# Kernel optimization log

Measured on AMD Instinct MI355X. Metric: run time of the kernel, lower is better.

The kernel has to match this reference:

```python
import jax, jax.numpy as jnp
import numpy as np

B, L, V = 4, 1024, 1280
N_EMBD, N_BIN, N_HID = 768, 8, 32
HORIZON = 10.0


def setup_inputs() -> dict:
    key = jax.random.key(0)
    k_h, k_age, k_gap, k_tgt, k_w1, k_w2 = jax.random.split(key, 6)
    h = jax.random.normal(k_h, (B, L, N_EMBD), dtype=jnp.float32)
    # ages increase along a trajectory; gaps in [0, 2) years
    age = jnp.sort(jax.random.uniform(k_age, (B, L), dtype=jnp.float32) * 80.0, axis=-1)
    targets_age = age + jax.random.uniform(k_gap, (B, L), dtype=jnp.float32) * 2.0
    delta_t = targets_age - age  # passed to forward but unused (as in torch source)
    targets = jax.random.randint(k_tgt, (B, L), 0, V, dtype=jnp.int32)
    W1 = jax.random.normal(k_w1, (N_EMBD, N_BIN * N_HID), dtype=jnp.float32) * 0.02
    W2 = jax.random.normal(k_w2, (N_HID, V), dtype=jnp.float32) * 0.02
    return {"h": h, "age": age, "targets_age": targets_age, "delta_t": delta_t,
            "targets": targets, "W1": W1, "W2": W2}


def _time_to_event(age, targets_age, targets):
    # delta_full[b,i,j] = targets_age[b,j] - age[b,i]
    delta_full = targets_age[:, None, :] - age[:, :, None]  # (B,L,L)
    i_idx = jnp.arange(L)
    # torch.triu(diagonal=0): keep targets[b,j] where j>=i, else 0
    upper = (i_idx[None, :] >= i_idx[:, None])  # (L,L) mask, col>=row
    targets_exp = jnp.where(upper[None, :, :], targets[:, None, :], 0)  # (B,L,L)
    # scatter-reduce amin of position index j into vocab slot targets_exp[b,i,j]
    # sentinel L plays the role of torch's -1 (min over srcs ignores it; src<=L-1)
    b_ix = jnp.arange(B)[:, None, None]
    r_ix = i_idx[None, :, None]
    src = jnp.broadcast_to(i_idx[None, None, :], (B, L, L)).astype(jnp.int32)
    token_index = jnp.full((B, L, V), L, dtype=jnp.int32)
    token_index = token_index.at[b_ix, r_ix, targets_exp].min(src)
    no_event = token_index == L
    token_index = jnp.where(no_event, L - 1, token_index)  # (B,L,V)
    tte = jnp.take_along_axis(delta_full, token_index, axis=-1)  # (B,L,V)
    return tte, no_event, token_index


def reference(h, age, targets_age, delta_t, targets, W1, W2):
    # two dense projections: (B,L,E) -> (B,L,n_bin,n_hid) -> (B,L,n_bin,V)
    x = jnp.einsum('ble,eo->blo', h, W1).reshape(B, L, N_BIN, N_HID)
    logits = jnp.einsum('blnh,hv->blnv', x, W2)
    tte, no_event, _ = _time_to_event(age, targets_age, targets)
    edges = jnp.linspace(0.0, HORIZON, N_BIN + 1)
    lo = edges[:-1][None, None, :, None]
    hi = edges[1:][None, None, :, None]
    t = tte[:, :, None, :]  # (B,L,1,V)
    censor_mask = ((t >= lo) & (t < hi)) | no_event[:, :, None, :]  # (B,L,n_bin,V)
    return logits, tte, censor_mask
```

## Files before the change

kernel.cpp:

```cpp
#include <hip/hip_runtime.h>
#include <hip/hip_bf16.h>

#define B_   4
#define L_   1024
#define V_   1280
#define NE_  768
#define NB_  8
#define NH_  32
#define NO_  (NB_*NH_)
#define BL_  (B_*L_)
#define M2_  (BL_*NB_)

typedef __attribute__((ext_vector_type(8))) short bf16x8;
typedef __attribute__((ext_vector_type(4))) float floatx4;

__device__ __forceinline__ unsigned short f2bf(float f) {
    unsigned int u = __float_as_uint(f);
    u += 0x7FFFu + ((u >> 16) & 1u);
    return (unsigned short)(u >> 16);
}

#define H4_N   (BL_*NE_/4)
#define W1T_N  (NO_*NE_)
#define W2T_N  (V_*NH_)
#define K0_TOT (H4_N + W1T_N + W2T_N)

__global__ __launch_bounds__(256) void k0_pack(const float* __restrict__ h,
                                               const float* __restrict__ W1,
                                               const float* __restrict__ W2,
                                               unsigned short* __restrict__ hb,
                                               unsigned short* __restrict__ W1T,
                                               unsigned short* __restrict__ W2T) {
    int id = blockIdx.x * 256 + threadIdx.x;
    if (id < H4_N) {
        float4 v = ((const float4*)h)[id];
        ushort4 o;
        o.x = f2bf(v.x); o.y = f2bf(v.y); o.z = f2bf(v.z); o.w = f2bf(v.w);
        ((ushort4*)hb)[id] = o;
    } else if (id < H4_N + W1T_N) {
        int j = id - H4_N;
        int o = j / NE_;
        int k = j - o * NE_;
        W1T[j] = f2bf(W1[(size_t)k * NO_ + o]);
    } else if (id < K0_TOT) {
        int j = id - H4_N - W1T_N;
        int v = j >> 5;
        int k = j & 31;
        W2T[j] = f2bf(W2[(size_t)k * V_ + v]);
    }
}

__global__ __launch_bounds__(256) void k1_gemm(const unsigned short* __restrict__ hb,
                                               const unsigned short* __restrict__ W1T,
                                               unsigned short* __restrict__ Xb) {
    __shared__ short A_lds[64][40];
    __shared__ short Bt_lds[64][40];

    const int t      = threadIdx.x;
    const int m0     = blockIdx.x * 64;
    const int n0     = blockIdx.y * 64;
    const int l      = t & 63;
    const int w      = t >> 6;
    const int lane15 = l & 15;
    const int quad   = l >> 4;

    const int srow = t >> 2;
    const int sq   = (t & 3) * 8;

    const unsigned short* aptr = hb  + (size_t)(m0 + srow) * NE_ + sq;
    const unsigned short* bptr = W1T + (size_t)(n0 + srow) * NE_ + sq;

    floatx4 acc[4];
#pragma unroll
    for (int i = 0; i < 4; ++i) acc[i] = (floatx4){0.f, 0.f, 0.f, 0.f};

    bf16x8 av = *(const bf16x8*)aptr;
    bf16x8 bv = *(const bf16x8*)bptr;

    for (int k0 = 0; k0 < NE_; k0 += 32) {
        __syncthreads();
        *(bf16x8*)&A_lds[srow][sq]  = av;
        *(bf16x8*)&Bt_lds[srow][sq] = bv;
        __syncthreads();
        if (k0 + 32 < NE_) {
            av = *(const bf16x8*)(aptr + k0 + 32);
            bv = *(const bf16x8*)(bptr + k0 + 32);
        }
        bf16x8 af = *(bf16x8*)&A_lds[w * 16 + lane15][quad * 8];
#pragma unroll
        for (int nt = 0; nt < 4; ++nt) {
            bf16x8 bf = *(bf16x8*)&Bt_lds[nt * 16 + lane15][quad * 8];
            acc[nt] = __builtin_amdgcn_mfma_f32_16x16x32_bf16(af, bf, acc[nt], 0, 0, 0);
        }
    }

    const int rbase = m0 + w * 16 + quad * 4;
#pragma unroll
    for (int nt = 0; nt < 4; ++nt)
#pragma unroll
        for (int r = 0; r < 4; ++r)
            Xb[(size_t)(rbase + r) * NO_ + n0 + nt * 16 + lane15] = f2bf(acc[nt][r]);
}

__global__ __launch_bounds__(256) void k2_logits(const unsigned short* __restrict__ Xb,
                                                 const unsigned short* __restrict__ W2T,
                                                 float* __restrict__ outL) {
    const int t      = threadIdx.x;
    const int m0     = blockIdx.x * 64;
    const int l      = t & 63;
    const int w      = t >> 6;
    const int lane15 = l & 15;
    const int quad   = l >> 4;

    const int m = m0 + w * 16 + lane15;
    const bf16x8 bfrag = *(const bf16x8*)(Xb + (size_t)m * NH_ + quad * 8);

    float* orow = outL + (size_t)m * V_ + quad * 4;
    const unsigned short* wrow = W2T + (size_t)lane15 * NH_ + quad * 8;

#pragma unroll 4
    for (int nt = 0; nt < V_ / 16; ++nt) {
        const bf16x8 afrag = *(const bf16x8*)(wrow + (size_t)nt * 16 * NH_);
        floatx4 c = (floatx4){0.f, 0.f, 0.f, 0.f};
        c = __builtin_amdgcn_mfma_f32_16x16x32_bf16(afrag, bfrag, c, 0, 0, 0);
        *(floatx4*)(orow + nt * 16) = c;
    }
}

#define K3_S 32
#define NCH  (L_/K3_S)

__global__ __launch_bounds__(256) void k3a_scan(const int* __restrict__ targets,
                                                int* __restrict__ sufocc) {
    __shared__ int tg[L_];
    const int t = threadIdx.x;
    const int v = blockIdx.x * 256 + t;
    const int b = blockIdx.z;

    for (int j = t; j < L_; j += 256) tg[j] = targets[(size_t)b * L_ + j];
    __syncthreads();

    int cur = L_;
    for (int i = L_ - 1; i >= 0; --i) {
        if (tg[i] == v) cur = i;
        if ((i & (K3_S - 1)) == 0)
            sufocc[(size_t)(b * NCH + (i >> 5)) * V_ + v] = cur;
    }
}

__global__ __launch_bounds__(256) void k3b_tte(const float* __restrict__ age,
                                               const float* __restrict__ tage,
                                               const int*   __restrict__ targets,
                                               const int*   __restrict__ sufocc,
                                               float* __restrict__ outT,
                                               float* __restrict__ outM) {
    __shared__ float ta[L_];
    __shared__ int   tg[K3_S];
    __shared__ float ag[K3_S];

    const int t      = threadIdx.x;
    const int v      = blockIdx.x * 256 + t;
    const int y      = blockIdx.y;
    const int istart = y * K3_S;
    const int b      = blockIdx.z;

    for (int j = t; j < L_; j += 256) ta[j] = tage[(size_t)b * L_ + j];
    if (t < K3_S) {
        tg[t] = targets[(size_t)b * L_ + istart + t];
        ag[t] = age[(size_t)b * L_ + istart + t];
    }
    __syncthreads();

    int cur = (y == NCH - 1) ? L_
                             : sufocc[(size_t)(b * NCH + y + 1) * V_ + v];

    for (int i = K3_S - 1; i >= 0; --i) {
        const int gi = istart + i;
        if (tg[i] == v) cur = gi;

        int idx = cur;
        if (v == 0 && gi >= 1) idx = 0;
        const bool noev = (idx == L_);
        const int  ic   = noev ? (L_ - 1) : idx;
        const float tte = ta[ic] - ag[i];

        outT[((size_t)(b * L_ + gi)) * V_ + v] = tte;

        const size_t mb = ((size_t)(b * L_ + gi)) * NB_ * V_ + v;
#pragma unroll
        for (int n = 0; n < NB_; ++n) {
            const float lo = n * 1.25f;
            const float hi = (n + 1) * 1.25f;
            const bool in_bin = (tte >= lo) && (tte < hi);
            outM[mb + (size_t)n * V_] = (in_bin || noev) ? 1.0f : 0.0f;
        }
    }
}

extern "C" void kernel_launch(void* const* d_in, const int* in_sizes, int n_in,
                              void* d_out, int out_size, void* d_ws, size_t ws_size,
                              hipStream_t stream) {
    const float* h       = (const float*)d_in[0];
    const float* age     = (const float*)d_in[1];
    const float* tage    = (const float*)d_in[2];
    const int*   targets = (const int*)  d_in[4];
    const float* W1      = (const float*)d_in[5];
    const float* W2      = (const float*)d_in[6];

    float* out  = (float*)d_out;
    float* outL = out;
    float* outT = out + (size_t)BL_ * NB_ * V_;
    float* outM = outT + (size_t)BL_ * V_;

    char* ws = (char*)d_ws;
    unsigned short* hb  = (unsigned short*)(ws);
    unsigned short* W1T = (unsigned short*)(ws + 6291456);
    unsigned short* W2T = (unsigned short*)(ws + 6291456 + 393216);
    unsigned short* Xb  = (unsigned short*)(ws + 6291456 + 393216 + 81920);
    int*            suf = (int*)           (ws + 6291456 + 393216 + 81920 + 2097152);

    k0_pack  <<<(K0_TOT + 255) / 256, 256, 0, stream>>>(h, W1, W2, hb, W1T, W2T);
    k1_gemm  <<<dim3(BL_/64, NO_/64), 256, 0, stream>>>(hb, W1T, Xb);
    k2_logits<<<M2_/64, 256, 0, stream>>>(Xb, W2T, outL);
    k3a_scan <<<dim3(V_/256, 1, B_), 256, 0, stream>>>(targets, suf);
    k3b_tte  <<<dim3(V_/256, L_/K3_S, B_), 256, 0, stream>>>(age, tage, targets, suf, outT, outM);
}
```

Measured before the change: 420.0 us.

## Fuse suffix scan into pack kernel and vectorize TTE/mask writes four-wide

Merges the per-vocab suffix-occurrence scan into the bf16 pack kernel as extra blocks, which removes one launch and lets the scan overlap with packing. It shrinks the chunk size from 32 to 8 rows, giving the tte kernel many more row-chunks. Each thread now handles four vocab entries with float4 stores for tte and the mask. The smaller chunks quadruple the suffix table writes, and the serial scan still runs inside the pack kernel, where it can lengthen that kernel's tail.

```diff
diff --git a/kernel.cpp b/kernel.cpp
--- a/kernel.cpp
+++ b/kernel.cpp
@@ -24,29 +24,54 @@
 #define W1T_N  (NO_*NE_)
 #define W2T_N  (V_*NH_)
 #define K0_TOT (H4_N + W1T_N + W2T_N)
-
-__global__ __launch_bounds__(256) void k0_pack(const float* __restrict__ h,
-                                               const float* __restrict__ W1,
-                                               const float* __restrict__ W2,
-                                               unsigned short* __restrict__ hb,
-                                               unsigned short* __restrict__ W1T,
-                                               unsigned short* __restrict__ W2T) {
-    int id = blockIdx.x * 256 + threadIdx.x;
-    if (id < H4_N) {
-        float4 v = ((const float4*)h)[id];
-        ushort4 o;
-        o.x = f2bf(v.x); o.y = f2bf(v.y); o.z = f2bf(v.z); o.w = f2bf(v.w);
-        ((ushort4*)hb)[id] = o;
-    } else if (id < H4_N + W1T_N) {
-        int j = id - H4_N;
-        int o = j / NE_;
-        int k = j - o * NE_;
-        W1T[j] = f2bf(W1[(size_t)k * NO_ + o]);
-    } else if (id < K0_TOT) {
-        int j = id - H4_N - W1T_N;
-        int v = j >> 5;
-        int k = j & 31;
-        W2T[j] = f2bf(W2[(size_t)k * V_ + v]);
+#define NPACK  ((K0_TOT + 255) / 256)
+#define NSCAN  ((V_/256) * B_)
+
+#define K3_S 8
+#define NCH  (L_/K3_S)
+
+__global__ __launch_bounds__(256) void k0_pack_scan(const float* __restrict__ h,
+                                                    const float* __restrict__ W1,
+                                                    const float* __restrict__ W2,
+                                                    const int*   __restrict__ targets,
+                                                    unsigned short* __restrict__ hb,
+                                                    unsigned short* __restrict__ W1T,
+                                                    unsigned short* __restrict__ W2T,
+                                                    int* __restrict__ sufocc) {
+    __shared__ int tg[L_];
+    if (blockIdx.x < NPACK) {
+        int id = blockIdx.x * 256 + threadIdx.x;
+        if (id < H4_N) {
+            float4 v = ((const float4*)h)[id];
+            ushort4 o;
+            o.x = f2bf(v.x); o.y = f2bf(v.y); o.z = f2bf(v.z); o.w = f2bf(v.w);
+            ((ushort4*)hb)[id] = o;
+        } else if (id < H4_N + W1T_N) {
+            int j = id - H4_N;
+            int o = j / NE_;
+            int k = j - o * NE_;
+            W1T[j] = f2bf(W1[(size_t)k * NO_ + o]);
+        } else if (id < K0_TOT) {
+            int j = id - H4_N - W1T_N;
+            int v = j >> 5;
+            int k = j & 31;
+            W2T[j] = f2bf(W2[(size_t)k * V_ + v]);
+        }
+    } else {
+        const int bscan = blockIdx.x - NPACK;
+        const int b     = bscan / (V_/256);
+        const int v     = (bscan % (V_/256)) * 256 + threadIdx.x;
+
+        for (int j = threadIdx.x; j < L_; j += 256)
+            tg[j] = targets[(size_t)b * L_ + j];
+        __syncthreads();
+
+        int cur = L_;
+        for (int i = L_ - 1; i >= 0; --i) {
+            if (tg[i] == v) cur = i;
+            if ((i & (K3_S - 1)) == 0)
+                sufocc[(size_t)(b * NCH + (i / K3_S)) * V_ + v] = cur;
+        }
     }
 }
 
@@ -127,28 +152,7 @@
     }
 }
 
-#define K3_S 32
-#define NCH  (L_/K3_S)
-
-__global__ __launch_bounds__(256) void k3a_scan(const int* __restrict__ targets,
-                                                int* __restrict__ sufocc) {
-    __shared__ int tg[L_];
-    const int t = threadIdx.x;
-    const int v = blockIdx.x * 256 + t;
-    const int b = blockIdx.z;
-
-    for (int j = t; j < L_; j += 256) tg[j] = targets[(size_t)b * L_ + j];
-    __syncthreads();
-
-    int cur = L_;
-    for (int i = L_ - 1; i >= 0; --i) {
-        if (tg[i] == v) cur = i;
-        if ((i & (K3_S - 1)) == 0)
-            sufocc[(size_t)(b * NCH + (i >> 5)) * V_ + v] = cur;
-    }
-}
-
-__global__ __launch_bounds__(256) void k3b_tte(const float* __restrict__ age,
+__global__ __launch_bounds__(320) void k3b_tte(const float* __restrict__ age,
                                                const float* __restrict__ tage,
                                                const int*   __restrict__ targets,
                                                const int*   __restrict__ sufocc,
@@ -159,40 +163,58 @@
     __shared__ float ag[K3_S];
 
     const int t      = threadIdx.x;
-    const int v      = blockIdx.x * 256 + t;
+    const int v4     = t * 4;
     const int y      = blockIdx.y;
     const int istart = y * K3_S;
     const int b      = blockIdx.z;
 
-    for (int j = t; j < L_; j += 256) ta[j] = tage[(size_t)b * L_ + j];
+    for (int j = t; j < L_; j += 320) ta[j] = tage[(size_t)b * L_ + j];
     if (t < K3_S) {
         tg[t] = targets[(size_t)b * L_ + istart + t];
         ag[t] = age[(size_t)b * L_ + istart + t];
     }
     __syncthreads();
 
-    int cur = (y == NCH - 1) ? L_
-                             : sufocc[(size_t)(b * NCH + y + 1) * V_ + v];
+    int cur0, cur1, cur2, cur3;
+    if (y == NCH - 1) {
+        cur0 = cur1 = cur2 = cur3 = L_;
+    } else {
+        const int4 cs = *(const int4*)&sufocc[(size_t)(b * NCH + y + 1) * V_ + v4];
+        cur0 = cs.x; cur1 = cs.y; cur2 = cs.z; cur3 = cs.w;
+    }
 
     for (int i = K3_S - 1; i >= 0; --i) {
         const int gi = istart + i;
-        if (tg[i] == v) cur = gi;
-
-        int idx = cur;
-        if (v == 0 && gi >= 1) idx = 0;
-        const bool noev = (idx == L_);
-        const int  ic   = noev ? (L_ - 1) : idx;
-        const float tte = ta[ic] - ag[i];
-
-        outT[((size_t)(b * L_ + gi)) * V_ + v] = tte;
-
-        const size_t mb = ((size_t)(b * L_ + gi)) * NB_ * V_ + v;
+        const int ti = tg[i];
+        if (ti == v4 + 0) cur0 = gi;
+        if (ti == v4 + 1) cur1 = gi;
+        if (ti == v4 + 2) cur2 = gi;
+        if (ti == v4 + 3) cur3 = gi;
+
+        int i0 = cur0, i1 = cur1, i2 = cur2, i3 = cur3;
+        if (v4 == 0 && gi >= 1) i0 = 0;
+
+        const bool nv0 = (i0 == L_), nv1 = (i1 == L_), nv2 = (i2 == L_), nv3 = (i3 == L_);
+        const float agi = ag[i];
+        const float t0 = ta[nv0 ? (L_ - 1) : i0] - agi;
+        const float t1 = ta[nv1 ? (L_ - 1) : i1] - agi;
+        const float t2 = ta[nv2 ? (L_ - 1) : i2] - agi;
+        const float t3 = ta[nv3 ? (L_ - 1) : i3] - agi;
+
+        float4 tt; tt.x = t0; tt.y = t1; tt.z = t2; tt.w = t3;
+        *(float4*)&outT[((size_t)(b * L_ + gi)) * V_ + v4] = tt;
+
+        const size_t mb = ((size_t)(b * L_ + gi)) * NB_ * V_ + v4;
 #pragma unroll
         for (int n = 0; n < NB_; ++n) {
             const float lo = n * 1.25f;
             const float hi = (n + 1) * 1.25f;
-            const bool in_bin = (tte >= lo) && (tte < hi);
-            outM[mb + (size_t)n * V_] = (in_bin || noev) ? 1.0f : 0.0f;
+            float4 mk;
+            mk.x = (((t0 >= lo) && (t0 < hi)) || nv0) ? 1.0f : 0.0f;
+            mk.y = (((t1 >= lo) && (t1 < hi)) || nv1) ? 1.0f : 0.0f;
+            mk.z = (((t2 >= lo) && (t2 < hi)) || nv2) ? 1.0f : 0.0f;
+            mk.w = (((t3 >= lo) && (t3 < hi)) || nv3) ? 1.0f : 0.0f;
+            *(float4*)&outM[mb + (size_t)n * V_] = mk;
         }
     }
 }
@@ -219,9 +241,8 @@
     unsigned short* Xb  = (unsigned short*)(ws + 6291456 + 393216 + 81920);
     int*            suf = (int*)           (ws + 6291456 + 393216 + 81920 + 2097152);
 
-    k0_pack  <<<(K0_TOT + 255) / 256, 256, 0, stream>>>(h, W1, W2, hb, W1T, W2T);
+    k0_pack_scan<<<NPACK + NSCAN, 256, 0, stream>>>(h, W1, W2, targets, hb, W1T, W2T, suf);
     k1_gemm  <<<dim3(BL_/64, NO_/64), 256, 0, stream>>>(hb, W1T, Xb);
     k2_logits<<<M2_/64, 256, 0, stream>>>(Xb, W2T, outL);
-    k3a_scan <<<dim3(V_/256, 1, B_), 256, 0, stream>>>(targets, suf);
-    k3b_tte  <<<dim3(V_/256, L_/K3_S, B_), 256, 0, stream>>>(age, tage, targets, suf, outT, outM);
-}
+    k3b_tte  <<<dim3(1, NCH, B_), 320, 0, stream>>>(age, tage, targets, suf, outT, outM);
+}
```

Measured after the change: 422.2 us, median of 2. Within noise of the previous version (+0.5%).
